# Performance work log

Hardware: AMD Instinct MI355X
Metric: run time of the kernel (lower is better)

## Reference

```python
import jax, jax.numpy as jnp
import numpy as np

D_MODEL = 1024
HEADS = 16
D_HEAD = D_MODEL // HEADS
B, S = 2, 2048
NEG_INF = -1e9
LN_EPS = 1e-6


def setup_inputs() -> dict:
    key = jax.random.key(0)
    ks = jax.random.split(key, 10)
    q = jax.random.normal(ks[0], (B, S, D_MODEL), dtype=jnp.float32)
    k = jax.random.normal(ks[1], (B, S, D_MODEL), dtype=jnp.float32)
    v = jax.random.normal(ks[2], (B, S, D_MODEL), dtype=jnp.float32)
    sen_len = jnp.clip(jax.random.randint(ks[3], (B,), 1, S + 1), 1, S).astype(jnp.int32)
    # xavier_uniform for square matrices: limit = sqrt(6/(fan_in+fan_out))
    lim = float(np.sqrt(6.0 / (D_MODEL + D_MODEL)))
    Wq = jax.random.uniform(ks[4], (D_MODEL, D_MODEL), jnp.float32, -lim, lim)
    Wk = jax.random.uniform(ks[5], (D_MODEL, D_MODEL), jnp.float32, -lim, lim)
    Wv = jax.random.uniform(ks[6], (D_MODEL, D_MODEL), jnp.float32, -lim, lim)
    Wo = jax.random.uniform(ks[7], (D_MODEL, D_MODEL), jnp.float32, -lim, lim)
    gamma = jnp.ones((D_MODEL,), jnp.float32)
    beta = jnp.zeros((D_MODEL,), jnp.float32)
    return {"q": q, "k": k, "v": v, "Wq": Wq, "Wk": Wk, "Wv": Wv,
            "Wo": Wo, "gamma": gamma, "beta": beta, "sen_len": sen_len}


def _split_heads(x):
    # (B,S,D) -> (B,H,S,d)
    b, s, _ = x.shape
    return x.reshape(b, s, HEADS, D_HEAD).transpose(0, 2, 1, 3)


def reference(q, k, v, Wq, Wk, Wv, Wo, gamma, beta, sen_len):
    residual = q
    # torch Linear (no bias): y = x @ W.T
    qh = _split_heads(q @ Wq.T)   # (B,H,S,d)
    kh = _split_heads(k @ Wk.T)
    vh = _split_heads(v @ Wv.T)

    scores = jnp.einsum("bhqd,bhkd->bhqk", qh, kh) / jnp.sqrt(jnp.float32(D_HEAD))
    pos = jnp.arange(S)
    causal = pos[:, None] >= pos[None, :]                       # (S,S) j<=i
    pad = pos[None, :] < sen_len[:, None]                       # (B,S) key within sentence
    valid = causal[None, None, :, :] & pad[:, None, None, :]    # (B,1,S,S)
    scores = jnp.where(valid, scores, NEG_INF)

    att = jax.nn.softmax(scores, axis=-1)
    ctx = jnp.einsum("bhqk,bhkd->bhqd", att, vh)                # (B,H,S,d)
    ctx = ctx.transpose(0, 2, 1, 3).reshape(q.shape[0], S, D_MODEL)

    out = ctx @ Wo.T
    # dropout is identity at inference
    out = out + residual
    mean = jnp.mean(out, axis=-1, keepdims=True)
    var = jnp.mean(jnp.square(out - mean), axis=-1, keepdims=True)
    out = (out - mean) / jnp.sqrt(var + LN_EPS) * gamma + beta
    return out
```

## Files before the change

### kernel.cpp

```cpp
#include <hip/hip_runtime.h>

#define SEQ 2048
#define DM  1024
#define NH  16
#define DH  64

typedef __attribute__((ext_vector_type(8))) __bf16 bf16x8;
typedef __attribute__((ext_vector_type(4))) float f32x4;

__device__ inline unsigned short f2b(float f) {
  union { float f; unsigned u; } a; a.f = f;
  unsigned u = a.u;
  u += 0x7fffu + ((u >> 16) & 1u);
  return (unsigned short)(u >> 16);
}

__device__ inline void glds16(const void* g, void* s) {
  __builtin_amdgcn_global_load_lds((const __attribute__((address_space(1))) void*)g,
                                   (__attribute__((address_space(3))) void*)s,
                                   16, 0, 0);
}

__global__ __launch_bounds__(256) void cvt_all(
    const float* __restrict__ q, const float* __restrict__ k,
    const float* __restrict__ v, const float* __restrict__ Wq,
    const float* __restrict__ Wk, const float* __restrict__ Wv,
    const float* __restrict__ Wo, unsigned short* __restrict__ qb,
    unsigned short* __restrict__ kb, unsigned short* __restrict__ vb,
    unsigned short* __restrict__ Wqb, unsigned short* __restrict__ Wkb,
    unsigned short* __restrict__ Wvb, unsigned short* __restrict__ Wob) {
  int blk = blockIdx.x;
  const float* src;
  unsigned short* dst;
  int rel;
  if (blk < 4096)        { src = q;  dst = qb;  rel = blk; }
  else if (blk < 8192)   { src = k;  dst = kb;  rel = blk - 4096; }
  else if (blk < 12288)  { src = v;  dst = vb;  rel = blk - 8192; }
  else if (blk < 13312)  { src = Wq; dst = Wqb; rel = blk - 12288; }
  else if (blk < 14336)  { src = Wk; dst = Wkb; rel = blk - 13312; }
  else if (blk < 15360)  { src = Wv; dst = Wvb; rel = blk - 14336; }
  else                   { src = Wo; dst = Wob; rel = blk - 15360; }
  int i = rel * 256 + threadIdx.x;
  float4 val = ((const float4*)src)[i];
  ushort4 o;
  o.x = f2b(val.x); o.y = f2b(val.y); o.z = f2b(val.z); o.w = f2b(val.w);
  ((ushort4*)dst)[i] = o;
}

template<int MODE>
__device__ inline void gemm_body(const unsigned short* __restrict__ A,
                                 const unsigned short* __restrict__ Bt,
                                 void* __restrict__ Cv, int N, int K,
                                 unsigned short* As, unsigned short* Bs,
                                 int mt, int nt) {
  const int tid = threadIdx.x;
  const int wave = tid >> 6, lane = tid & 63;
  const int quad = lane >> 4, l16 = lane & 15;
  const int m0 = mt * 128, n0 = nt * 128;
  const int wm = (wave >> 1) * 64, wn = (wave & 1) * 64;
  const int srow = lane >> 3, scol = (lane & 7) * 8;

  f32x4 acc[4][4];
#pragma unroll
  for (int i = 0; i < 4; i++)
#pragma unroll
    for (int j = 0; j < 4; j++) acc[i][j] = (f32x4)0.f;

  for (int k0 = 0; k0 < K; k0 += 64) {
#pragma unroll
    for (int c = 0; c < 4; c++) {
      int inst = wave * 4 + c;
      int row = inst * 8 + srow;
      glds16(A + (size_t)(m0 + row) * K + k0 + scol, &As[inst * 512]);
      glds16(Bt + (size_t)(n0 + row) * K + k0 + scol, &Bs[inst * 512]);
    }
    __syncthreads();
#pragma unroll
    for (int ks = 0; ks < 2; ks++) {
      bf16x8 af[4], bfr[4];
#pragma unroll
      for (int i = 0; i < 4; i++)
        af[i] = *(const bf16x8*)&As[(wm + i * 16 + l16) * 64 + ks * 32 + quad * 8];
#pragma unroll
      for (int j = 0; j < 4; j++)
        bfr[j] = *(const bf16x8*)&Bs[(wn + j * 16 + l16) * 64 + ks * 32 + quad * 8];
#pragma unroll
      for (int i = 0; i < 4; i++)
#pragma unroll
        for (int j = 0; j < 4; j++)
          acc[i][j] = __builtin_amdgcn_mfma_f32_16x16x32_bf16(af[i], bfr[j],
                                                              acc[i][j], 0, 0, 0);
    }
    __syncthreads();
  }
#pragma unroll
  for (int i = 0; i < 4; i++)
#pragma unroll
    for (int j = 0; j < 4; j++)
#pragma unroll
      for (int r = 0; r < 4; r++) {
        int row = m0 + wm + i * 16 + quad * 4 + r;
        int col = n0 + wn + j * 16 + l16;
        if (MODE == 0) {
          ((unsigned short*)Cv)[(size_t)row * N + col] = f2b(acc[i][j][r]);
        } else if (MODE == 1) {
          ((float*)Cv)[(size_t)row * N + col] = acc[i][j][r];
        } else if (MODE == 2) {
          int b = row >> 11, s = row & 2047;
          int h = col >> 6, d = col & 63;
          size_t off = (((size_t)(b * NH + h) * 32 + (s >> 6)) * 8 +
                        ((s >> 4) & 3) * 2 + (d >> 5)) * 512 +
                       (((d >> 3) & 3) * 16 + (s & 15)) * 8 + (d & 7);
          ((unsigned short*)Cv)[off] = f2b(acc[i][j][r]);
        } else {
          int b = row >> 11, s = row & 2047, jj = s & 63;
          int h = col >> 6, d = col & 63;
          size_t off = (((size_t)(b * NH + h) * 32 + (s >> 6)) * 8 +
                        (jj >> 5) * 4 + (d >> 4)) * 512 +
                       (((jj >> 3) & 3) * 16 + (d & 15)) * 8 + (jj & 7);
          ((unsigned short*)Cv)[off] = f2b(acc[i][j][r]);
        }
      }
}

__global__ __launch_bounds__(256) void gemm_qkv(
    const unsigned short* __restrict__ A0, const unsigned short* __restrict__ A1,
    const unsigned short* __restrict__ A2, const unsigned short* __restrict__ B0,
    const unsigned short* __restrict__ B1, const unsigned short* __restrict__ B2,
    unsigned short* __restrict__ C0, unsigned short* __restrict__ C1,
    unsigned short* __restrict__ C2) {
  __shared__ unsigned short As[128 * 64];
  __shared__ unsigned short Bs[128 * 64];
  const int mt = blockIdx.x, nt = blockIdx.y;
  if (blockIdx.z == 0)      gemm_body<0>(A0, B0, (void*)C0, DM, DM, As, Bs, mt, nt);
  else if (blockIdx.z == 1) gemm_body<2>(A1, B1, (void*)C1, DM, DM, As, Bs, mt, nt);
  else                      gemm_body<3>(A2, B2, (void*)C2, DM, DM, As, Bs, mt, nt);
}

__global__ __launch_bounds__(256) void gemm_out(const unsigned short* __restrict__ A,
                                                const unsigned short* __restrict__ Bt,
                                                float* __restrict__ C) {
  __shared__ unsigned short As[128 * 64];
  __shared__ unsigned short Bs[128 * 64];
  gemm_body<1>(A, Bt, (void*)C, DM, DM, As, Bs, blockIdx.x, blockIdx.y);
}

__global__ __launch_bounds__(64) void attn_kernel(const unsigned short* __restrict__ Qp,
                                                  const unsigned short* __restrict__ Ksw,
                                                  const unsigned short* __restrict__ Vsw,
                                                  const int* __restrict__ sen_len,
                                                  unsigned short* __restrict__ ctx) {
  __shared__ unsigned int Pl[2][16 * 36];

  const int lane = threadIdx.x;
  const int quad = lane >> 4, l16 = lane & 15;
  const int bh = blockIdx.x, b = bh >> 4, h = bh & 15;
  const int pair = 63 - (int)blockIdx.y;
  const int qt0 = pair * 2;
  const int slen = sen_len[b];

  int qrow[2];
  qrow[0] = qt0 * 16 + l16;
  qrow[1] = qt0 * 16 + 16 + l16;

  bf16x8 qf[2][2];
#pragma unroll
  for (int sub = 0; sub < 2; sub++) {
    const size_t qbase = ((size_t)b * SEQ + qrow[sub]) * DM + h * DH;
    qf[sub][0] = *(const bf16x8*)(Qp + qbase + quad * 8);
    qf[sub][1] = *(const bf16x8*)(Qp + qbase + 32 + quad * 8);
  }

  const unsigned short* kbase = Ksw + (size_t)bh * 32 * 4096 + lane * 8;
  const unsigned short* vbase = Vsw + (size_t)bh * 32 * 4096 + lane * 8;

  int jend = qt0 * 16 + 32;
  if (slen < jend) jend = slen;
  const int nch = (jend + 63) >> 6;

  float m[2] = {-1e30f, -1e30f};
  float lsum[2] = {0.f, 0.f};
  f32x4 o[2][4];
#pragma unroll
  for (int sub = 0; sub < 2; sub++)
#pragma unroll
    for (int i = 0; i < 4; i++) o[sub][i] = (f32x4)0.f;

  for (int c = 0; c < nch; ++c) {
    const int j0 = c * 64;
    bf16x8 ka[4][2], vf[2][4];
#pragma unroll
    for (int fi = 0; fi < 8; fi++)
      ka[fi >> 1][fi & 1] = *(const bf16x8*)(kbase + (size_t)c * 4096 + fi * 512);
#pragma unroll
    for (int fi = 0; fi < 8; fi++)
      vf[fi >> 2][fi & 3] = *(const bf16x8*)(vbase + (size_t)c * 4096 + fi * 512);

#pragma unroll
    for (int sub = 0; sub < 2; sub++) {
      f32x4 sacc[4];
#pragma unroll
      for (int kt = 0; kt < 4; kt++) sacc[kt] = (f32x4)0.f;
#pragma unroll
      for (int kt = 0; kt < 4; kt++) {
        sacc[kt] = __builtin_amdgcn_mfma_f32_16x16x32_bf16(ka[kt][0], qf[sub][0],
                                                           sacc[kt], 0, 0, 0);
        sacc[kt] = __builtin_amdgcn_mfma_f32_16x16x32_bf16(ka[kt][1], qf[sub][1],
                                                           sacc[kt], 0, 0, 0);
      }
      float cmax = -1e30f;
#pragma unroll
      for (int kt = 0; kt < 4; kt++)
#pragma unroll
        for (int r = 0; r < 4; r++) {
          int j = j0 + kt * 16 + quad * 4 + r;
          float v = (j <= qrow[sub] && j < slen) ? sacc[kt][r] * 0.125f : -1e30f;
          sacc[kt][r] = v;
          cmax = fmaxf(cmax, v);
        }
      cmax = fmaxf(cmax, __shfl_xor(cmax, 16));
      cmax = fmaxf(cmax, __shfl_xor(cmax, 32));
      float mnew = fmaxf(m[sub], cmax);
      float alpha = __expf(m[sub] - mnew);
      float psum = 0.f;
#pragma unroll
      for (int kt = 0; kt < 4; kt++)
#pragma unroll
        for (int rp = 0; rp < 2; rp++) {
          float p0 = __expf(sacc[kt][2 * rp] - mnew);
          float p1 = __expf(sacc[kt][2 * rp + 1] - mnew);
          psum += p0 + p1;
          Pl[sub][l16 * 36 + kt * 8 + quad * 2 + rp] =
              (unsigned)f2b(p0) | ((unsigned)f2b(p1) << 16);
        }
      psum += __shfl_xor(psum, 16);
      psum += __shfl_xor(psum, 32);
      lsum[sub] = lsum[sub] * alpha + psum;
      m[sub] = mnew;
#pragma unroll
      for (int r = 0; r < 4; r++) {
        float ar = __shfl(alpha, quad * 4 + r);
#pragma unroll
        for (int ni = 0; ni < 4; ni++) o[sub][ni][r] *= ar;
      }
      const unsigned short* Pw16 = (const unsigned short*)&Pl[sub][0];
#pragma unroll
      for (int ko = 0; ko < 2; ko++) {
        bf16x8 pf = *(const bf16x8*)&Pw16[l16 * 72 + ko * 32 + quad * 8];
#pragma unroll
        for (int ni = 0; ni < 4; ni++)
          o[sub][ni] = __builtin_amdgcn_mfma_f32_16x16x32_bf16(pf, vf[ko][ni],
                                                               o[sub][ni], 0, 0, 0);
      }
    }
  }

#pragma unroll
  for (int sub = 0; sub < 2; sub++)
#pragma unroll
    for (int r = 0; r < 4; r++) {
      float lr = __shfl(lsum[sub], quad * 4 + r);
      float inv = 1.0f / lr;
      int row = qt0 * 16 + sub * 16 + quad * 4 + r;
#pragma unroll
      for (int ni = 0; ni < 4; ni++) {
        float v = o[sub][ni][r] * inv;
        ctx[((size_t)b * SEQ + row) * DM + h * DH + ni * 16 + l16] = f2b(v);
      }
    }
}

__global__ __launch_bounds__(256) void ln_kernel(const float* __restrict__ xp,
                                                 const float* __restrict__ resid,
                                                 const float* __restrict__ gamma,
                                                 const float* __restrict__ beta,
                                                 float* __restrict__ out) {
  const int row = blockIdx.x;
  const int tid = threadIdx.x;
  const size_t base = (size_t)row * DM + tid * 4;
  float4 x = *(const float4*)(xp + base);
  float4 rv = *(const float4*)(resid + base);
  x.x += rv.x; x.y += rv.y; x.z += rv.z; x.w += rv.w;
  float s = x.x + x.y + x.z + x.w;
  float s2 = x.x * x.x + x.y * x.y + x.z * x.z + x.w * x.w;
#pragma unroll
  for (int off = 1; off < 64; off <<= 1) {
    s += __shfl_xor(s, off);
    s2 += __shfl_xor(s2, off);
  }
  __shared__ float sm[4], sm2[4];
  const int wave = tid >> 6, lane = tid & 63;
  if (lane == 0) { sm[wave] = s; sm2[wave] = s2; }
  __syncthreads();
  s = sm[0] + sm[1] + sm[2] + sm[3];
  s2 = sm2[0] + sm2[1] + sm2[2] + sm2[3];
  float mean = s * (1.f / 1024.f);
  float var = s2 * (1.f / 1024.f) - mean * mean;
  float rstd = rsqrtf(var + 1e-6f);
  float4 g = *(const float4*)(gamma + tid * 4);
  float4 bt = *(const float4*)(beta + tid * 4);
  float4 o;
  o.x = (x.x - mean) * rstd * g.x + bt.x;
  o.y = (x.y - mean) * rstd * g.y + bt.y;
  o.z = (x.z - mean) * rstd * g.z + bt.z;
  o.w = (x.w - mean) * rstd * g.w + bt.w;
  *(float4*)(out + base) = o;
}

extern "C" void kernel_launch(void* const* d_in, const int* in_sizes, int n_in,
                              void* d_out, int out_size, void* d_ws, size_t ws_size,
                              hipStream_t stream) {
  const float* q     = (const float*)d_in[0];
  const float* k     = (const float*)d_in[1];
  const float* v     = (const float*)d_in[2];
  const float* Wq    = (const float*)d_in[3];
  const float* Wk    = (const float*)d_in[4];
  const float* Wv    = (const float*)d_in[5];
  const float* Wo    = (const float*)d_in[6];
  const float* gamma = (const float*)d_in[7];
  const float* beta  = (const float*)d_in[8];
  const int* sen_len = (const int*)d_in[9];
  float* out = (float*)d_out;

  char* ws = (char*)d_ws;
  const size_t MB = (size_t)1 << 20;
  if (ws_size < 64 * MB) return;
  unsigned short* qb  = (unsigned short*)(ws + 0 * MB);
  unsigned short* kb  = (unsigned short*)(ws + 8 * MB);
  unsigned short* vb  = (unsigned short*)(ws + 16 * MB);
  unsigned short* Wqb = (unsigned short*)(ws + 24 * MB);
  unsigned short* Wkb = (unsigned short*)(ws + 26 * MB);
  unsigned short* Wvb = (unsigned short*)(ws + 28 * MB);
  unsigned short* Wob = (unsigned short*)(ws + 30 * MB);
  unsigned short* Qp  = (unsigned short*)(ws + 32 * MB);
  unsigned short* Ksw = (unsigned short*)(ws + 40 * MB);
  unsigned short* Vsw = (unsigned short*)(ws + 48 * MB);
  unsigned short* ctx = (unsigned short*)(ws + 56 * MB);
  float* outp = (float*)(ws + 8 * MB);

  cvt_all<<<16384, 256, 0, stream>>>(q, k, v, Wq, Wk, Wv, Wo,
                                     qb, kb, vb, Wqb, Wkb, Wvb, Wob);

  gemm_qkv<<<dim3(32, 8, 3), 256, 0, stream>>>(qb, kb, vb, Wqb, Wkb, Wvb,
                                               Qp, Ksw, Vsw);

  attn_kernel<<<dim3(32, 64), 64, 0, stream>>>(Qp, Ksw, Vsw, sen_len, ctx);

  gemm_out<<<dim3(32, 8), 256, 0, stream>>>(ctx, Wob, outp);

  ln_kernel<<<4096, 256, 0, stream>>>(outp, q, gamma, beta, out);
}
```

Measured before the change: 252.2 us.

## Split attention KV chunks across four waves and merge partial softmax states in LDS

```diff
diff --git a/kernel.cpp b/kernel.cpp
--- a/kernel.cpp
+++ b/kernel.cpp
@@ -145,14 +145,17 @@
   gemm_body<1>(A, Bt, (void*)C, DM, DM, As, Bs, blockIdx.x, blockIdx.y);
 }
 
-__global__ __launch_bounds__(64) void attn_kernel(const unsigned short* __restrict__ Qp,
-                                                  const unsigned short* __restrict__ Ksw,
-                                                  const unsigned short* __restrict__ Vsw,
-                                                  const int* __restrict__ sen_len,
-                                                  unsigned short* __restrict__ ctx) {
-  __shared__ unsigned int Pl[2][16 * 36];
-
-  const int lane = threadIdx.x;
+__global__ __launch_bounds__(256) void attn_kernel(const unsigned short* __restrict__ Qp,
+                                                   const unsigned short* __restrict__ Ksw,
+                                                   const unsigned short* __restrict__ Vsw,
+                                                   const int* __restrict__ sen_len,
+                                                   unsigned short* __restrict__ ctx) {
+  __shared__ unsigned int Pl[4][16 * 36];
+  __shared__ float oS[2][64][33];
+  __shared__ float stS[2][2][16][2];
+
+  const int tid = threadIdx.x;
+  const int wave = tid >> 6, lane = tid & 63;
   const int quad = lane >> 4, l16 = lane & 15;
   const int bh = blockIdx.x, b = bh >> 4, h = bh & 15;
   const int pair = 63 - (int)blockIdx.y;
@@ -177,6 +180,8 @@
   int jend = qt0 * 16 + 32;
   if (slen < jend) jend = slen;
   const int nch = (jend + 63) >> 6;
+  const int c0 = (wave * nch) >> 2;
+  const int c1 = ((wave + 1) * nch) >> 2;
 
   float m[2] = {-1e30f, -1e30f};
   float lsum[2] = {0.f, 0.f};
@@ -186,7 +191,7 @@
 #pragma unroll
     for (int i = 0; i < 4; i++) o[sub][i] = (f32x4)0.f;
 
-  for (int c = 0; c < nch; ++c) {
+  for (int c = c0; c < c1; ++c) {
     const int j0 = c * 64;
     bf16x8 ka[4][2], vf[2][4];
 #pragma unroll
@@ -230,7 +235,7 @@
           float p0 = __expf(sacc[kt][2 * rp] - mnew);
           float p1 = __expf(sacc[kt][2 * rp + 1] - mnew);
           psum += p0 + p1;
-          Pl[sub][l16 * 36 + kt * 8 + quad * 2 + rp] =
+          Pl[wave][l16 * 36 + kt * 8 + quad * 2 + rp] =
               (unsigned)f2b(p0) | ((unsigned)f2b(p1) << 16);
         }
       psum += __shfl_xor(psum, 16);
@@ -243,7 +248,7 @@
 #pragma unroll
         for (int ni = 0; ni < 4; ni++) o[sub][ni][r] *= ar;
       }
-      const unsigned short* Pw16 = (const unsigned short*)&Pl[sub][0];
+      const unsigned short* Pw16 = (const unsigned short*)&Pl[wave][0];
 #pragma unroll
       for (int ko = 0; ko < 2; ko++) {
         bf16x8 pf = *(const bf16x8*)&Pw16[l16 * 72 + ko * 32 + quad * 8];
@@ -255,19 +260,68 @@
     }
   }
 
-#pragma unroll
-  for (int sub = 0; sub < 2; sub++)
-#pragma unroll
-    for (int r = 0; r < 4; r++) {
-      float lr = __shfl(lsum[sub], quad * 4 + r);
-      float inv = 1.0f / lr;
-      int row = qt0 * 16 + sub * 16 + quad * 4 + r;
-#pragma unroll
-      for (int ni = 0; ni < 4; ni++) {
-        float v = o[sub][ni][r] * inv;
-        ctx[((size_t)b * SEQ + row) * DM + h * DH + ni * 16 + l16] = f2b(v);
+  auto publish = [&](int slot) {
+#pragma unroll
+    for (int sub = 0; sub < 2; sub++)
+#pragma unroll
+      for (int ni = 0; ni < 4; ni++)
+#pragma unroll
+        for (int r = 0; r < 4; r++)
+          oS[slot][lane][sub * 16 + ni * 4 + r] = o[sub][ni][r];
+    if (quad == 0) {
+#pragma unroll
+      for (int sub = 0; sub < 2; sub++) {
+        stS[slot][sub][l16][0] = m[sub];
+        stS[slot][sub][l16][1] = lsum[sub];
       }
     }
+  };
+  auto mergeSlot = [&](int slot) {
+#pragma unroll
+    for (int sub = 0; sub < 2; sub++) {
+      float ms = stS[slot][sub][l16][0];
+      float ls = stS[slot][sub][l16][1];
+      float M = fmaxf(m[sub], ms);
+      float aL = __expf(m[sub] - M);
+      float aS = __expf(ms - M);
+      lsum[sub] = aL * lsum[sub] + aS * ls;
+      m[sub] = M;
+#pragma unroll
+      for (int r = 0; r < 4; r++) {
+        float aLr = __shfl(aL, quad * 4 + r);
+        float aSr = __shfl(aS, quad * 4 + r);
+#pragma unroll
+        for (int ni = 0; ni < 4; ni++)
+          o[sub][ni][r] = aLr * o[sub][ni][r] +
+                          aSr * oS[slot][lane][sub * 16 + ni * 4 + r];
+      }
+    }
+  };
+
+  if (wave == 1) publish(0);
+  if (wave == 3) publish(1);
+  __syncthreads();
+  if (wave == 0) mergeSlot(0);
+  if (wave == 2) mergeSlot(1);
+  __syncthreads();
+  if (wave == 2) publish(0);
+  __syncthreads();
+  if (wave == 0) {
+    mergeSlot(0);
+#pragma unroll
+    for (int sub = 0; sub < 2; sub++)
+#pragma unroll
+      for (int r = 0; r < 4; r++) {
+        float lr = __shfl(lsum[sub], quad * 4 + r);
+        float inv = 1.0f / lr;
+        int row = qt0 * 16 + sub * 16 + quad * 4 + r;
+#pragma unroll
+        for (int ni = 0; ni < 4; ni++) {
+          float v = o[sub][ni][r] * inv;
+          ctx[((size_t)b * SEQ + row) * DM + h * DH + ni * 16 + l16] = f2b(v);
+        }
+      }
+  }
 }
 
 __global__ __launch_bounds__(256) void ln_kernel(const float* __restrict__ xp,
@@ -344,7 +398,7 @@
   gemm_qkv<<<dim3(32, 8, 3), 256, 0, stream>>>(qb, kb, vb, Wqb, Wkb, Wvb,
                                                Qp, Ksw, Vsw);
 
-  attn_kernel<<<dim3(32, 64), 64, 0, stream>>>(Qp, Ksw, Vsw, sen_len, ctx);
+  attn_kernel<<<dim3(32, 64), 256, 0, stream>>>(Qp, Ksw, Vsw, sen_len, ctx);
 
   gemm_out<<<dim3(32, 8), 256, 0, stream>>>(ctx, Wob, outp);
 
```

Result: no change. 248.6 us (-1.5%).
